# Kernel tuning notes

Hardware: AMD Instinct MI355X
Metric: run time of the kernel (lower is better)

## Reference

```python
import jax, jax.numpy as jnp
import numpy as np

BINS = 128

def _histograms(x, bins):
    # x: [B, C, H, W], values histogrammed over [0, 1] per (b, c) slice,
    # matching torch.histc(min=0, max=1): out-of-range values ignored,
    # values exactly equal to max go in the last bin.
    B, C, H, W = x.shape
    xf = x.reshape(B * C, H * W)
    idx = jnp.floor(xf * bins).astype(jnp.int32)
    idx = jnp.where(xf >= 1.0, bins - 1, idx)  # x == max -> last bin
    in_range = (xf >= 0.0) & (xf <= 1.0)
    # offset each (b,c) slice into its own bin range, route invalid to a trash bin
    offs = jnp.arange(B * C, dtype=jnp.int32)[:, None] * bins
    flat_idx = jnp.where(in_range, idx + offs, B * C * bins)
    counts = jnp.zeros(B * C * bins + 1, dtype=x.dtype).at[flat_idx.ravel()].add(1.0)
    hist = counts[: B * C * bins].reshape(B, C * bins)
    return hist / (H * W)


def setup_inputs() -> dict:
    key = jax.random.key(0)
    k1, k2, k3 = jax.random.split(key, 3)
    x = jax.random.uniform(k1, (64, 3, 512, 512), dtype=jnp.float32)
    W = jax.random.normal(k2, (128, 3 * BINS), dtype=jnp.float32) * (1.0 / np.sqrt(3 * BINS))
    b = jax.random.normal(k3, (128,), dtype=jnp.float32) * 0.01
    return {"x": x, "W": W, "b": b}


def reference(x, W, b):
    feats = _histograms(x, BINS)          # [B, 3*bins]
    out = feats @ W.T + b                 # [B, 128]
    return jax.nn.relu(out)
```

## Files before the change

### kernel.cpp

```cpp
#include <hip/hip_runtime.h>


#define BINS 128
#define NSLICE 192
#define SLICE_ELEMS 262144
#define CHUNKS 8
#define CHUNK_ELEMS (SLICE_ELEMS / CHUNKS)
#define THREADS 256
#define WAVES 4
#define TOTAL_BLOCKS (NSLICE * CHUNKS)

__global__ __launch_bounds__(THREADS) void hist_part(const float* __restrict__ x,
                                                     unsigned int* __restrict__ part32) {
    __shared__ unsigned int lh[WAVES][BINS];

    const int bid  = blockIdx.x;
    const int tid  = threadIdx.x;
    const int wave = tid >> 6;

    for (int i = tid; i < WAVES * BINS; i += THREADS)
        ((unsigned int*)lh)[i] = 0u;
    __syncthreads();

    const float4* __restrict__ x4 = (const float4*)x;
    const int n4    = CHUNK_ELEMS >> 2;
    const int base4 = bid * n4;
#pragma unroll 8
    for (int i = tid; i < n4; i += THREADS) {
        float4 v = x4[base4 + i];
        float vv[4] = {v.x, v.y, v.z, v.w};
#pragma unroll
        for (int j = 0; j < 4; ++j) {
            float f = vv[j];
            if (f >= 0.0f && f <= 1.0f) {
                int idx = (int)(f * (float)BINS);
                if (idx > BINS - 1) idx = BINS - 1;
                atomicAdd(&lh[wave][idx], 1u);
            }
        }
    }
    __syncthreads();

    if (tid < BINS / 2) {
        uint2 a0 = ((const uint2*)lh[0])[tid];
        uint2 a1 = ((const uint2*)lh[1])[tid];
        uint2 a2 = ((const uint2*)lh[2])[tid];
        uint2 a3 = ((const uint2*)lh[3])[tid];
        unsigned int s0 = a0.x + a1.x + a2.x + a3.x;
        unsigned int s1 = a0.y + a1.y + a2.y + a3.y;
        part32[bid * (BINS / 2) + tid] = s0 | (s1 << 16);
    }
}

__global__ __launch_bounds__(THREADS) void reduce_gemm(const unsigned int* __restrict__ part32,
                                                       const float* __restrict__ W,
                                                       const float* __restrict__ bias,
                                                       float* __restrict__ out) {
    const int b   = blockIdx.x >> 1;
    const int g   = blockIdx.x & 1;
    const int tid = threadIdx.x;

    __shared__ float h[3 * BINS];
    __shared__ float psum[THREADS];

    const float inv = 1.0f / (float)SLICE_ELEMS;
    if (tid < 192) {
        const int slice = b * 3 + (tid >> 6);
        const int pi    = tid & 63;
        const unsigned int* __restrict__ p =
            part32 + (size_t)slice * CHUNKS * (BINS / 2) + pi;
        unsigned int s0 = 0, s1 = 0;
#pragma unroll
        for (int c = 0; c < CHUNKS; ++c) {
            unsigned int u = p[c * (BINS / 2)];
            s0 += u & 0xFFFFu;
            s1 += u >> 16;
        }
        h[2 * tid]     = (float)s0 * inv;
        h[2 * tid + 1] = (float)s1 * inv;
    }
    __syncthreads();

    const int o = tid & 63;
    const int q = tid >> 6;
    const int n = g * 64 + o;
    float acc = 0.0f;
    const float4* __restrict__ Wr = (const float4*)(W + n * 3 * BINS + q * 96);
    const float* __restrict__ hh  = h + q * 96;
#pragma unroll
    for (int k4 = 0; k4 < 24; ++k4) {
        float4 w = Wr[k4];
        acc += w.x * hh[4 * k4 + 0] + w.y * hh[4 * k4 + 1] +
               w.z * hh[4 * k4 + 2] + w.w * hh[4 * k4 + 3];
    }
    psum[tid] = acc;
    __syncthreads();
    if (tid < 64)
        out[b * BINS + n] = fmaxf(psum[o] + psum[64 + o] + psum[128 + o] +
                                  psum[192 + o] + bias[n], 0.0f);
}


__global__ __launch_bounds__(THREADS) void hist_atomic(const float* __restrict__ x,
                                                       unsigned int* __restrict__ ghist) {
    __shared__ unsigned int lh[WAVES][BINS];
    const int bid = blockIdx.x, tid = threadIdx.x, wave = tid >> 6;
    const int slice = bid / CHUNKS;
    for (int i = tid; i < WAVES * BINS; i += THREADS)
        ((unsigned int*)lh)[i] = 0u;
    __syncthreads();
    const float4* __restrict__ x4 = (const float4*)x;
    const int n4 = CHUNK_ELEMS >> 2, base4 = bid * n4;
#pragma unroll 4
    for (int i = tid; i < n4; i += THREADS) {
        float4 v = x4[base4 + i];
        float vv[4] = {v.x, v.y, v.z, v.w};
#pragma unroll
        for (int j = 0; j < 4; ++j) {
            float f = vv[j];
            if (f >= 0.0f && f <= 1.0f) {
                int idx = (int)(f * (float)BINS);
                if (idx > BINS - 1) idx = BINS - 1;
                atomicAdd(&lh[wave][idx], 1u);
            }
        }
    }
    __syncthreads();
    if (tid < BINS) {
        unsigned int s = lh[0][tid] + lh[1][tid] + lh[2][tid] + lh[3][tid];
        atomicAdd(&ghist[slice * BINS + tid], s);
    }
}

__global__ __launch_bounds__(128) void gemm_atomic(const unsigned int* __restrict__ ghist,
                                                   const float* __restrict__ W,
                                                   const float* __restrict__ bias,
                                                   float* __restrict__ out) {
    const int b = blockIdx.x, n = threadIdx.x;
    __shared__ float h[3 * BINS];
    const float inv = 1.0f / (float)SLICE_ELEMS;
    for (int k = n; k < 3 * BINS; k += 128)
        h[k] = (float)ghist[b * 3 * BINS + k] * inv;
    __syncthreads();
    float acc = bias[n];
    const float4* __restrict__ Wr = (const float4*)(W + n * 3 * BINS);
#pragma unroll 8
    for (int k4 = 0; k4 < 96; ++k4) {
        float4 w = Wr[k4];
        acc += w.x * h[4 * k4 + 0] + w.y * h[4 * k4 + 1] +
               w.z * h[4 * k4 + 2] + w.w * h[4 * k4 + 3];
    }
    out[b * 128 + n] = fmaxf(acc, 0.0f);
}

extern "C" void kernel_launch(void* const* d_in, const int* in_sizes, int n_in,
                              void* d_out, int out_size, void* d_ws, size_t ws_size,
                              hipStream_t stream) {
    const float* x    = (const float*)d_in[0];
    const float* W    = (const float*)d_in[1];
    const float* bias = (const float*)d_in[2];
    float* out        = (float*)d_out;

    const size_t part_bytes = (size_t)TOTAL_BLOCKS * (BINS / 2) * sizeof(unsigned int);
    if (ws_size >= part_bytes) {
        unsigned int* part32 = (unsigned int*)d_ws;
        hist_part<<<TOTAL_BLOCKS, THREADS, 0, stream>>>(x, part32);
        reduce_gemm<<<128, THREADS, 0, stream>>>(part32, W, bias, out);
    } else {
        unsigned int* ghist = (unsigned int*)d_ws;
        hipMemsetAsync(ghist, 0, NSLICE * BINS * sizeof(unsigned int), stream);
        hist_atomic<<<TOTAL_BLOCKS, THREADS, 0, stream>>>(x, ghist);
        gemm_atomic<<<64, 128, 0, stream>>>(ghist, W, bias, out);
    }
}
```

Baseline: 38.99 us.

## Fuse histogram and GEMM into one kernel with last-block ticket handoff

Merges the histogram and reduce+GEMM kernels into a single launch. Each block publishes its partial histogram, takes a ticket from a global atomic counter, and the last 128 blocks to finish spin until every block is done, then run the reduce and GEMM. This removes one kernel launch and the inter-kernel gap, but adds a memset launch for the counter, a spin-wait, and relaxed-atomic memory-ordering risk. The old atomic fallback path is dropped.

New measurement: 64.81 us. 1.66x slower.

```diff
diff --git a/kernel.cpp b/kernel.cpp
--- a/kernel.cpp
+++ b/kernel.cpp
@@ -9,10 +9,18 @@
 #define THREADS 256
 #define WAVES 4
 #define TOTAL_BLOCKS (NSLICE * CHUNKS)
-
-__global__ __launch_bounds__(THREADS) void hist_part(const float* __restrict__ x,
-                                                     unsigned int* __restrict__ part32) {
+#define GEMM_BLOCKS 128
+#define HIST_ONLY (TOTAL_BLOCKS - GEMM_BLOCKS)
+#define CTL_BYTES 256
+
+__global__ __launch_bounds__(THREADS) void fused_hist_gemm(
+        const float* __restrict__ x, const float* __restrict__ W,
+        const float* __restrict__ bias, float* __restrict__ out,
+        unsigned int* __restrict__ ctl, unsigned int* __restrict__ part32) {
     __shared__ unsigned int lh[WAVES][BINS];
+    __shared__ unsigned int s_ticket;
+    __shared__ float h[3 * BINS];
+    __shared__ float psum[THREADS];
 
     const int bid  = blockIdx.x;
     const int tid  = threadIdx.x;
@@ -41,6 +49,99 @@
     }
     __syncthreads();
 
+    if (tid < BINS / 2) {
+        uint2 a0 = ((const uint2*)lh[0])[tid];
+        uint2 a1 = ((const uint2*)lh[1])[tid];
+        uint2 a2 = ((const uint2*)lh[2])[tid];
+        uint2 a3 = ((const uint2*)lh[3])[tid];
+        unsigned int s0 = a0.x + a1.x + a2.x + a3.x;
+        unsigned int s1 = a0.y + a1.y + a2.y + a3.y;
+        __hip_atomic_store(&part32[bid * (BINS / 2) + tid], s0 | (s1 << 16),
+                           __ATOMIC_RELAXED, __HIP_MEMORY_SCOPE_AGENT);
+    }
+    __syncthreads();
+    asm volatile("s_waitcnt vmcnt(0)" ::: "memory");
+    if (tid == 0)
+        s_ticket = __hip_atomic_fetch_add(&ctl[0], 1u, __ATOMIC_RELAXED,
+                                          __HIP_MEMORY_SCOPE_AGENT);
+    __syncthreads();
+    const unsigned int ticket = s_ticket;
+    if (ticket < HIST_ONLY) return;
+
+    const int w = (int)(ticket - HIST_ONLY);
+    const int b = w >> 1;
+    const int g = w & 1;
+
+    if (tid == 0) {
+        while (__hip_atomic_load(&ctl[0], __ATOMIC_RELAXED,
+                                 __HIP_MEMORY_SCOPE_AGENT) < TOTAL_BLOCKS)
+            __builtin_amdgcn_s_sleep(2);
+    }
+    __syncthreads();
+
+    const float inv = 1.0f / (float)SLICE_ELEMS;
+    if (tid < 192) {
+        const int slice = b * 3 + (tid >> 6);
+        const int pi    = tid & 63;
+        const unsigned int* p = part32 + (size_t)slice * CHUNKS * (BINS / 2) + pi;
+        unsigned int s0 = 0, s1 = 0;
+#pragma unroll
+        for (int c = 0; c < CHUNKS; ++c) {
+            unsigned int u = __hip_atomic_load(&p[c * (BINS / 2)],
+                                               __ATOMIC_RELAXED,
+                                               __HIP_MEMORY_SCOPE_AGENT);
+            s0 += u & 0xFFFFu;
+            s1 += u >> 16;
+        }
+        h[2 * tid]     = (float)s0 * inv;
+        h[2 * tid + 1] = (float)s1 * inv;
+    }
+    __syncthreads();
+
+    const int o = tid & 63;
+    const int q = tid >> 6;
+    const int n = g * 64 + o;
+    float acc = 0.0f;
+    const float4* __restrict__ Wr = (const float4*)(W + n * 3 * BINS + q * 96);
+    const float* __restrict__ hh  = h + q * 96;
+#pragma unroll
+    for (int k4 = 0; k4 < 24; ++k4) {
+        float4 wv = Wr[k4];
+        acc += wv.x * hh[4 * k4 + 0] + wv.y * hh[4 * k4 + 1] +
+               wv.z * hh[4 * k4 + 2] + wv.w * hh[4 * k4 + 3];
+    }
+    psum[tid] = acc;
+    __syncthreads();
+    if (tid < 64)
+        out[b * BINS + n] = fmaxf(psum[o] + psum[64 + o] + psum[128 + o] +
+                                  psum[192 + o] + bias[n], 0.0f);
+}
+
+
+__global__ __launch_bounds__(THREADS) void hist_part(const float* __restrict__ x,
+                                                     unsigned int* __restrict__ part32) {
+    __shared__ unsigned int lh[WAVES][BINS];
+    const int bid = blockIdx.x, tid = threadIdx.x, wave = tid >> 6;
+    for (int i = tid; i < WAVES * BINS; i += THREADS)
+        ((unsigned int*)lh)[i] = 0u;
+    __syncthreads();
+    const float4* __restrict__ x4 = (const float4*)x;
+    const int n4 = CHUNK_ELEMS >> 2, base4 = bid * n4;
+#pragma unroll 8
+    for (int i = tid; i < n4; i += THREADS) {
+        float4 v = x4[base4 + i];
+        float vv[4] = {v.x, v.y, v.z, v.w};
+#pragma unroll
+        for (int j = 0; j < 4; ++j) {
+            float f = vv[j];
+            if (f >= 0.0f && f <= 1.0f) {
+                int idx = (int)(f * (float)BINS);
+                if (idx > BINS - 1) idx = BINS - 1;
+                atomicAdd(&lh[wave][idx], 1u);
+            }
+        }
+    }
+    __syncthreads();
     if (tid < BINS / 2) {
         uint2 a0 = ((const uint2*)lh[0])[tid];
         uint2 a1 = ((const uint2*)lh[1])[tid];
@@ -56,13 +157,9 @@
                                                        const float* __restrict__ W,
                                                        const float* __restrict__ bias,
                                                        float* __restrict__ out) {
-    const int b   = blockIdx.x >> 1;
-    const int g   = blockIdx.x & 1;
-    const int tid = threadIdx.x;
-
+    const int b = blockIdx.x >> 1, g = blockIdx.x & 1, tid = threadIdx.x;
     __shared__ float h[3 * BINS];
     __shared__ float psum[THREADS];
-
     const float inv = 1.0f / (float)SLICE_ELEMS;
     if (tid < 192) {
         const int slice = b * 3 + (tid >> 6);
@@ -80,77 +177,21 @@
         h[2 * tid + 1] = (float)s1 * inv;
     }
     __syncthreads();
-
-    const int o = tid & 63;
-    const int q = tid >> 6;
-    const int n = g * 64 + o;
+    const int o = tid & 63, q = tid >> 6, n = g * 64 + o;
     float acc = 0.0f;
     const float4* __restrict__ Wr = (const float4*)(W + n * 3 * BINS + q * 96);
     const float* __restrict__ hh  = h + q * 96;
 #pragma unroll
     for (int k4 = 0; k4 < 24; ++k4) {
-        float4 w = Wr[k4];
-        acc += w.x * hh[4 * k4 + 0] + w.y * hh[4 * k4 + 1] +
-               w.z * hh[4 * k4 + 2] + w.w * hh[4 * k4 + 3];
+        float4 wv = Wr[k4];
+        acc += wv.x * hh[4 * k4 + 0] + wv.y * hh[4 * k4 + 1] +
+               wv.z * hh[4 * k4 + 2] + wv.w * hh[4 * k4 + 3];
     }
     psum[tid] = acc;
     __syncthreads();
     if (tid < 64)
         out[b * BINS + n] = fmaxf(psum[o] + psum[64 + o] + psum[128 + o] +
                                   psum[192 + o] + bias[n], 0.0f);
-}
-
-
-__global__ __launch_bounds__(THREADS) void hist_atomic(const float* __restrict__ x,
-                                                       unsigned int* __restrict__ ghist) {
-    __shared__ unsigned int lh[WAVES][BINS];
-    const int bid = blockIdx.x, tid = threadIdx.x, wave = tid >> 6;
-    const int slice = bid / CHUNKS;
-    for (int i = tid; i < WAVES * BINS; i += THREADS)
-        ((unsigned int*)lh)[i] = 0u;
-    __syncthreads();
-    const float4* __restrict__ x4 = (const float4*)x;
-    const int n4 = CHUNK_ELEMS >> 2, base4 = bid * n4;
-#pragma unroll 4
-    for (int i = tid; i < n4; i += THREADS) {
-        float4 v = x4[base4 + i];
-        float vv[4] = {v.x, v.y, v.z, v.w};
-#pragma unroll
-        for (int j = 0; j < 4; ++j) {
-            float f = vv[j];
-            if (f >= 0.0f && f <= 1.0f) {
-                int idx = (int)(f * (float)BINS);
-                if (idx > BINS - 1) idx = BINS - 1;
-                atomicAdd(&lh[wave][idx], 1u);
-            }
-        }
-    }
-    __syncthreads();
-    if (tid < BINS) {
-        unsigned int s = lh[0][tid] + lh[1][tid] + lh[2][tid] + lh[3][tid];
-        atomicAdd(&ghist[slice * BINS + tid], s);
-    }
-}
-
-__global__ __launch_bounds__(128) void gemm_atomic(const unsigned int* __restrict__ ghist,
-                                                   const float* __restrict__ W,
-                                                   const float* __restrict__ bias,
-                                                   float* __restrict__ out) {
-    const int b = blockIdx.x, n = threadIdx.x;
-    __shared__ float h[3 * BINS];
-    const float inv = 1.0f / (float)SLICE_ELEMS;
-    for (int k = n; k < 3 * BINS; k += 128)
-        h[k] = (float)ghist[b * 3 * BINS + k] * inv;
-    __syncthreads();
-    float acc = bias[n];
-    const float4* __restrict__ Wr = (const float4*)(W + n * 3 * BINS);
-#pragma unroll 8
-    for (int k4 = 0; k4 < 96; ++k4) {
-        float4 w = Wr[k4];
-        acc += w.x * h[4 * k4 + 0] + w.y * h[4 * k4 + 1] +
-               w.z * h[4 * k4 + 2] + w.w * h[4 * k4 + 3];
-    }
-    out[b * 128 + n] = fmaxf(acc, 0.0f);
 }
 
 extern "C" void kernel_launch(void* const* d_in, const int* in_sizes, int n_in,
@@ -162,14 +203,14 @@
     float* out        = (float*)d_out;
 
     const size_t part_bytes = (size_t)TOTAL_BLOCKS * (BINS / 2) * sizeof(unsigned int);
-    if (ws_size >= part_bytes) {
+    if (ws_size >= CTL_BYTES + part_bytes) {
+        unsigned int* ctl    = (unsigned int*)d_ws;
+        unsigned int* part32 = (unsigned int*)((char*)d_ws + CTL_BYTES);
+        hipMemsetAsync(ctl, 0, 8, stream);
+        fused_hist_gemm<<<TOTAL_BLOCKS, THREADS, 0, stream>>>(x, W, bias, out, ctl, part32);
+    } else if (ws_size >= part_bytes) {
         unsigned int* part32 = (unsigned int*)d_ws;
         hist_part<<<TOTAL_BLOCKS, THREADS, 0, stream>>>(x, part32);
         reduce_gemm<<<128, THREADS, 0, stream>>>(part32, W, bias, out);
-    } else {
-        unsigned int* ghist = (unsigned int*)d_ws;
-        hipMemsetAsync(ghist, 0, NSLICE * BINS * sizeof(unsigned int), stream);
-        hist_atomic<<<TOTAL_BLOCKS, THREADS, 0, stream>>>(x, ghist);
-        gemm_atomic<<<64, 128, 0, stream>>>(ghist, W, bias, out);
-    }
-}
+    }
+}
```
